# Kernel tuning notes

Hardware: AMD Instinct MI355X
Metric: run time of the kernel (lower is better)

Reference implementation:

```python
import jax, jax.numpy as jnp
import numpy as np

D_MODEL = 2048
NUM_HEADS = 16
D_K = D_MODEL // NUM_HEADS  # 128
MAX_SEQ_LEN = 4096
THETA = 10000.0
BATCH = 2
SEQ = 2048


def _trunc_normal(key, shape, std):
    # approximate trunc_normal_(mean=0, std, a=-3std, b=3std)
    return jnp.clip(jax.random.normal(key, shape) * std, -3 * std, 3 * std)


def setup_inputs() -> dict:
    key = jax.random.key(0)
    k0, k1, k2, k3, k4 = jax.random.split(key, 5)
    std = 2.0 / (D_MODEL + D_MODEL) ** 0.5
    in_features = jax.random.normal(k0, (BATCH, SEQ, D_MODEL), dtype=jnp.float32)
    token_positions = jnp.arange(SEQ, dtype=jnp.int64 if jax.config.jax_enable_x64 else jnp.int32)
    wq = _trunc_normal(k1, (D_MODEL, D_MODEL), std)
    wk = _trunc_normal(k2, (D_MODEL, D_MODEL), std)
    wv = _trunc_normal(k3, (D_MODEL, D_MODEL), std)
    wo = _trunc_normal(k4, (D_MODEL, D_MODEL), std)
    return {"in_features": in_features, "token_positions": token_positions,
            "wq": wq, "wk": wk, "wv": wv, "wo": wo}


def _rope(x, token_positions):
    # x: [b, h, s, d_k]; token_positions: [s]
    freqs = 1.0 / THETA ** (jnp.arange(0, D_K, 2, dtype=jnp.float32) / D_K)  # [d_k/2]
    angles = token_positions.astype(jnp.float32)[:, None] * freqs[None, :]   # [s, d_k/2]
    sin = jnp.sin(angles)
    cos = jnp.cos(angles)
    x1 = x[..., ::2]
    x2 = x[..., 1::2]
    rot = jnp.stack([x1 * cos - x2 * sin, x1 * sin + x2 * cos], axis=-1)  # [b,h,s,d_k/2,2]
    return rot.reshape(x.shape)


def reference(in_features, token_positions, wq, wk, wv, wo):
    b, s, _ = in_features.shape
    # projections: weight is [d_out, d_in]
    q = jnp.einsum('oi,bsi->bso', wq, in_features)
    k = jnp.einsum('oi,bsi->bso', wk, in_features)
    v = jnp.einsum('oi,bsi->bso', wv, in_features)
    # split heads: [b, s, h*d] -> [b, h, s, d]
    def split(t):
        return t.reshape(b, s, NUM_HEADS, D_K).transpose(0, 2, 1, 3)
    q, k, v = split(q), split(k), split(v)
    q = _rope(q, token_positions)
    k = _rope(k, token_positions)
    scores = jnp.einsum('bhqd,bhkd->bhqk', q, k) / jnp.sqrt(jnp.float32(D_K))
    causal = jnp.tril(jnp.ones((s, s), dtype=bool))
    scores = jnp.where(causal, scores, -jnp.inf)
    attn = jax.nn.softmax(scores, axis=-1)
    out = jnp.einsum('bhqk,bhkd->bhqd', attn, v)
    out = out.transpose(0, 2, 1, 3).reshape(b, s, D_MODEL)
    return jnp.einsum('oi,bsi->bso', wo, out)
```

## Files before the change

### kernel.cpp

```cpp
#include <hip/hip_runtime.h>
#include <cstdint>

typedef unsigned short u16;
typedef __attribute__((ext_vector_type(8))) short short8;
typedef __attribute__((ext_vector_type(4))) float f32x4;
typedef __attribute__((ext_vector_type(16))) float f32x16;
typedef __attribute__((ext_vector_type(2))) unsigned int uint2v;

#define D_MODEL 2048
#define NHEAD   16
#define DK      128
#define SEQQ    2048
#define BATCH   2
#define MTOT    (BATCH*SEQQ)

#define FENCE() asm volatile("" ::: "memory")
#define BARRIER() do { FENCE(); __builtin_amdgcn_s_barrier(); FENCE(); } while (0)

__device__ __forceinline__ u16 f2b(float f) {
  union { float f; uint32_t u; } c; c.f = f;
  uint32_t u = c.u;
  u += 0x7fffu + ((u >> 16) & 1u);
  return (u16)(u >> 16);
}
__device__ __forceinline__ float b2f(u16 h) {
  union { uint32_t u; float f; } c; c.u = ((uint32_t)h) << 16;
  return c.f;
}

__device__ __forceinline__ void gload_lds16(const void* g, void* l) {
  __builtin_amdgcn_global_load_lds(
      (const __attribute__((address_space(1))) void*)(uintptr_t)g,
      (__attribute__((address_space(3))) void*)(uint32_t)(uintptr_t)l,
      16, 0, 0);
}

__global__ __launch_bounds__(256) void cvt_bf16(const float* __restrict__ src,
                                                u16* __restrict__ dst, int n4) {
  int i = blockIdx.x * 256 + threadIdx.x;
  if (i >= n4) return;
  float4 v = ((const float4*)src)[i];
  union { u16 s[4]; uint64_t q; } o;
  o.s[0] = f2b(v.x); o.s[1] = f2b(v.y); o.s[2] = f2b(v.z); o.s[3] = f2b(v.w);
  ((uint64_t*)dst)[i] = o.q;
}

__global__ __launch_bounds__(256) void cvt_w(const float* __restrict__ wq,
                                             const float* __restrict__ wk,
                                             const float* __restrict__ wv,
                                             const float* __restrict__ wo,
                                             u16* __restrict__ Wqkv,
                                             u16* __restrict__ Wob) {
  int i = blockIdx.x * 256 + threadIdx.x;
  int which = i >> 20, j = i & 1048575;
  const float* src = (which == 0) ? wq : (which == 1) ? wk : (which == 2) ? wv : wo;
  u16* dst = (which < 3) ? (Wqkv + (size_t)which * 4194304) : Wob;
  float4 v = ((const float4*)src)[j];
  union { u16 s[4]; uint64_t q; } o;
  o.s[0] = f2b(v.x); o.s[1] = f2b(v.y); o.s[2] = f2b(v.z); o.s[3] = f2b(v.w);
  ((uint64_t*)dst)[j] = o.q;
}

template<int MODE>
__global__ __launch_bounds__(512) void gemm8(const u16* __restrict__ A,
                                             const u16* __restrict__ B,
                                             u16* __restrict__ Cq, u16* __restrict__ Ck,
                                             u16* __restrict__ Vt, float* __restrict__ Cf,
                                             int cpx) {
  __shared__ __align__(16) u16 As[3][128 * 64];
  __shared__ __align__(16) u16 Bs[3][256 * 64];
  const int tid = threadIdx.x;
  const int wave = tid >> 6, lane = tid & 63;
  const int l15 = lane & 15, l4 = lane >> 4;
  const int wr = wave >> 2, wc = wave & 3;
  const int wg = ((int)blockIdx.x & 7) * cpx + ((int)blockIdx.x >> 3);
  const int bm = wg & 31, bn = wg >> 5;
  const int row0 = bm * 128, col0 = bn * 256;

  const u16* asrc[2]; const u16* bsrc[4];
  {
    const int r = tid >> 3, c8 = tid & 7;
#pragma unroll
    for (int p = 0; p < 2; ++p) {
      int row = p * 64 + r;
      asrc[p] = A + (size_t)(row0 + row) * 2048 + ((c8 ^ (row & 7)) << 3);
    }
#pragma unroll
    for (int p = 0; p < 4; ++p) {
      int row = p * 64 + r;
      bsrc[p] = B + (size_t)(col0 + row) * 2048 + ((c8 ^ (row & 7)) << 3);
    }
  }
  const int ldst = wave * 512 + lane * 8;

  int aoff[4][2], boff[4][2];
#pragma unroll
  for (int m = 0; m < 4; ++m) {
    int row = wr * 64 + m * 16 + l15;
#pragma unroll
    for (int ks = 0; ks < 2; ++ks)
      aoff[m][ks] = row * 64 + (((ks * 4 + l4) ^ (l15 & 7)) << 3);
  }
#pragma unroll
  for (int n = 0; n < 4; ++n) {
    int row = wc * 64 + n * 16 + l15;
#pragma unroll
    for (int ks = 0; ks < 2; ++ks)
      boff[n][ks] = row * 64 + (((ks * 4 + l4) ^ (l15 & 7)) << 3);
  }

  f32x4 acc[4][4] = {};

#define STAGE0(slot, kt) do { \
    gload_lds16(asrc[0] + ((kt) << 6), &As[slot][0 * 4096 + ldst]); \
    gload_lds16(asrc[1] + ((kt) << 6), &As[slot][1 * 4096 + ldst]); \
    gload_lds16(bsrc[0] + ((kt) << 6), &Bs[slot][0 * 4096 + ldst]); \
  } while (0)
#define STAGE1(slot, kt) do { \
    gload_lds16(bsrc[1] + ((kt) << 6), &Bs[slot][1 * 4096 + ldst]); \
    gload_lds16(bsrc[2] + ((kt) << 6), &Bs[slot][2 * 4096 + ldst]); \
    gload_lds16(bsrc[3] + ((kt) << 6), &Bs[slot][3 * 4096 + ldst]); \
  } while (0)

  STAGE0(0, 0); STAGE1(0, 0);
  STAGE0(1, 1); STAGE1(1, 1);
  asm volatile("s_waitcnt vmcnt(6)" ::: "memory");
  BARRIER();

  int slot = 0;
  for (int t = 0; t < 32; ++t) {
    const int slot2 = slot ? slot - 1 : 2;
    const bool pf = (t + 2 < 32);
    short8 af[4], bf[4];
#pragma unroll
    for (int m = 0; m < 4; ++m) af[m] = *(const short8*)&As[slot][aoff[m][0]];
#pragma unroll
    for (int n = 0; n < 4; ++n) bf[n] = *(const short8*)&Bs[slot][boff[n][0]];
    if (pf) STAGE0(slot2, t + 2);
    BARRIER();
    __builtin_amdgcn_s_setprio(1);
#pragma unroll
    for (int m = 0; m < 4; ++m)
#pragma unroll
      for (int n = 0; n < 4; ++n)
        acc[m][n] = __builtin_amdgcn_mfma_f32_16x16x32_bf16(af[m], bf[n], acc[m][n], 0, 0, 0);
    __builtin_amdgcn_s_setprio(0);
    BARRIER();
#pragma unroll
    for (int m = 0; m < 4; ++m) af[m] = *(const short8*)&As[slot][aoff[m][1]];
#pragma unroll
    for (int n = 0; n < 4; ++n) bf[n] = *(const short8*)&Bs[slot][boff[n][1]];
    if (pf) STAGE1(slot2, t + 2);
    BARRIER();
    __builtin_amdgcn_s_setprio(1);
#pragma unroll
    for (int m = 0; m < 4; ++m)
#pragma unroll
      for (int n = 0; n < 4; ++n)
        acc[m][n] = __builtin_amdgcn_mfma_f32_16x16x32_bf16(af[m], bf[n], acc[m][n], 0, 0, 0);
    __builtin_amdgcn_s_setprio(0);
    if (pf) asm volatile("s_waitcnt vmcnt(6)" ::: "memory");
    else    asm volatile("s_waitcnt vmcnt(0)" ::: "memory");
    BARRIER();
    slot = (slot == 2) ? 0 : slot + 1;
  }
#undef STAGE0
#undef STAGE1

#pragma unroll
  for (int m = 0; m < 4; ++m) {
    const int row = row0 + wr * 64 + m * 16 + l4 * 4;
#pragma unroll
    for (int n = 0; n < 4; ++n) {
      const int col = wc * 64 + n * 16 + l15;
      if (MODE == 1) {
#pragma unroll
        for (int r = 0; r < 4; ++r)
          Cf[(size_t)(row + r) * 2048 + col0 + col] = acc[m][n][r];
      } else {
        const int region = col0 >> 11;
        const int col2 = (col0 & 2047) + col;
        if (region < 2) {
          u16* Cx = region ? Ck : Cq;
#pragma unroll
          for (int r = 0; r < 4; ++r)
            Cx[(size_t)(row + r) * 2048 + col2] = f2b(acc[m][n][r]);
        } else {
          union { u16 h4[4]; uint64_t q; } pk;
#pragma unroll
          for (int r = 0; r < 4; ++r) pk.h4[r] = f2b(acc[m][n][r]);
          const int bb = row >> 11, ss = row & 2047;
          const int hh = col2 >> 7, dd = col2 & 127;
          *(uint64_t*)&Vt[((size_t)((bb << 4) + hh) * 128 + dd) * 2048 + ss] = pk.q;
        }
      }
    }
  }
}

__global__ __launch_bounds__(256) void rope_qk(u16* __restrict__ Qb, u16* __restrict__ Kb,
                                               const int* __restrict__ pos) {
  int p = blockIdx.x * 256 + threadIdx.x;
  u16* X = (p >> 22) ? Kb : Qb;
  int pp = p & 4194303;
  int m = pp >> 10, j2 = pp & 1023;
  int h = j2 >> 6, j = j2 & 63;
  int s = m & (SEQQ - 1);
  float fp = (float)pos[s];
  float freq = exp2f((float)j * -0.20762050593046014f);
  float ang = fp * freq;
  float sn, cs;
  sincosf(ang, &sn, &cs);
  u16* px = X + (size_t)m * D_MODEL + h * DK + 2 * j;
  uint32_t pair = *(uint32_t*)px;
  float x1 = b2f((u16)(pair & 0xffff)), x2 = b2f((u16)(pair >> 16));
  u16 r1 = f2b(x1 * cs - x2 * sn);
  u16 r2 = f2b(x1 * sn + x2 * cs);
  *(uint32_t*)px = (uint32_t)r1 | ((uint32_t)r2 << 16);
}

__global__ __launch_bounds__(256) void attn_fwd(const u16* __restrict__ Q,
                                                const u16* __restrict__ Kg,
                                                const u16* __restrict__ Vt,
                                                u16* __restrict__ O) {
  __shared__ __align__(16) u16 Klds[2][64 * 128];
  __shared__ __align__(16) u16 Vlds[2][128 * 64];
  const int tid = threadIdx.x, wave = tid >> 6, lane = tid & 63;
  const int l31 = lane & 31, l5 = lane >> 5;
  const int bh = blockIdx.x;
  const int bxr = 15 - (int)blockIdx.y;
  const int b = bh >> 4, h = bh & 15;
  const int q0 = bxr * 128, qw = q0 + wave * 32;
  const float qscale = 0.1275174470974136f;

  short8 bq[8];
  {
    const u16* Qp = Q + (size_t)(b * SEQQ + qw + l31) * D_MODEL + h * DK + l5 * 8;
#pragma unroll
    for (int dt = 0; dt < 8; ++dt) {
      short8 raw = *(const short8*)(Qp + dt * 16);
#pragma unroll
      for (int j = 0; j < 8; ++j) raw[j] = (short)f2b(b2f((u16)raw[j]) * qscale);
      bq[dt] = raw;
    }
  }
  asm volatile("s_waitcnt vmcnt(0)" ::: "memory");

  f32x16 facc[4] = {};
  float mrun = -1e30f, lpart = 0.f;

  const u16* Kbase = Kg + (size_t)b * SEQQ * D_MODEL + h * DK;
  const u16* Vbase = Vt + (size_t)bh * DK * SEQQ;
  const u16* ksrc[4]; const u16* vsrc[4];
#pragma unroll
  for (int g = 0; g < 4; ++g) {
    int kr = g * 16 + (tid >> 4);
    int kc = ((tid & 15) * 8) ^ ((kr & 7) << 3);
    ksrc[g] = Kbase + (size_t)kr * D_MODEL + kc;
    int vr = g * 32 + (tid >> 3);
    int vc = ((tid & 7) * 8) ^ ((vr & 7) << 3);
    vsrc[g] = Vbase + (size_t)vr * SEQQ + vc;
  }
  const int dstoff = tid * 8;
  const int nkt = 2 * (bxr + 1);

#pragma unroll
  for (int g = 0; g < 4; ++g) { gload_lds16(ksrc[g], &Klds[0][g * 2048 + dstoff]); ksrc[g] += (size_t)64 * D_MODEL; }
#pragma unroll
  for (int g = 0; g < 4; ++g) { gload_lds16(vsrc[g], &Vlds[0][g * 2048 + dstoff]); vsrc[g] += 64; }

  for (int kt = 0; kt < nkt; ++kt) {
    const int k0 = kt * 64, cur = kt & 1;
    asm volatile("s_waitcnt vmcnt(0)" ::: "memory");
    BARRIER();
    if (kt + 1 < nkt) {
#pragma unroll
      for (int g = 0; g < 4; ++g) { gload_lds16(ksrc[g], &Klds[cur ^ 1][g * 2048 + dstoff]); ksrc[g] += (size_t)64 * D_MODEL; }
#pragma unroll
      for (int g = 0; g < 4; ++g) { gload_lds16(vsrc[g], &Vlds[cur ^ 1][g * 2048 + dstoff]); vsrc[g] += 64; }
    }
    if (k0 > qw + 31) continue;

    const u16* Kl = Klds[cur];
    const u16* Vl = Vlds[cur];

    f32x16 st0 = {}, st1 = {};
    __builtin_amdgcn_s_setprio(1);
#pragma unroll
    for (int dt = 0; dt < 8; ++dt) {
      const int ch = ((2 * dt + l5) ^ (l31 & 7)) * 8;
      short8 ak0 = *(const short8*)&Kl[l31 * 128 + ch];
      short8 ak1 = *(const short8*)&Kl[(32 + l31) * 128 + ch];
      st0 = __builtin_amdgcn_mfma_f32_32x32x16_bf16(ak0, bq[dt], st0, 0, 0, 0);
      st1 = __builtin_amdgcn_mfma_f32_32x32x16_bf16(ak1, bq[dt], st1, 0, 0, 0);
    }
    __builtin_amdgcn_s_setprio(0);

    if (k0 + 63 > qw) {
      const int qm = qw + l31 - k0 - 4 * l5;
#pragma unroll
      for (int r = 0; r < 16; ++r) {
        const int kc0 = (r & 3) + 8 * (r >> 2);
        st0[r] = (kc0 > qm) ? -1e30f : st0[r];
        st1[r] = (kc0 + 32 > qm) ? -1e30f : st1[r];
      }
    }

    float mx[8];
#pragma unroll
    for (int r = 0; r < 8; ++r) mx[r] = fmaxf(fmaxf(st0[r], st0[r + 8]), fmaxf(st1[r], st1[r + 8]));
    float m = fmaxf(fmaxf(fmaxf(mx[0], mx[1]), fmaxf(mx[2], mx[3])),
                    fmaxf(fmaxf(mx[4], mx[5]), fmaxf(mx[6], mx[7])));
    {
      uint2v sw = __builtin_amdgcn_permlane32_swap(__float_as_uint(m), __float_as_uint(m), false, false);
      m = fmaxf(__uint_as_float(sw.x), __uint_as_float(sw.y));
    }
    const float mn = fmaxf(mrun, m);
    const float al = exp2f(mrun - mn);
    mrun = mn;
    float ps = 0.f;
#pragma unroll
    for (int r = 0; r < 16; ++r) { float p = exp2f(st0[r] - mn); st0[r] = p; ps += p; }
#pragma unroll
    for (int r = 0; r < 16; ++r) { float p = exp2f(st1[r] - mn); st1[r] = p; ps += p; }
    lpart = lpart * al + ps;
#pragma unroll
    for (int db = 0; db < 4; ++db) facc[db] *= al;

    short8 pa[4];
#pragma unroll
    for (int ks2 = 0; ks2 < 2; ++ks2) {
#pragma unroll
      for (int t0 = 0; t0 < 2; ++t0) {
        uint32_t c0w0, c0w1, c1w0, c1w1;
        if (ks2 == 0) {
          asm("v_cvt_pk_bf16_f32 %0, %1, %2" : "=v"(c0w0) : "v"(st0[8 * t0 + 0]), "v"(st0[8 * t0 + 1]));
          asm("v_cvt_pk_bf16_f32 %0, %1, %2" : "=v"(c0w1) : "v"(st0[8 * t0 + 2]), "v"(st0[8 * t0 + 3]));
          asm("v_cvt_pk_bf16_f32 %0, %1, %2" : "=v"(c1w0) : "v"(st0[8 * t0 + 4]), "v"(st0[8 * t0 + 5]));
          asm("v_cvt_pk_bf16_f32 %0, %1, %2" : "=v"(c1w1) : "v"(st0[8 * t0 + 6]), "v"(st0[8 * t0 + 7]));
        } else {
          asm("v_cvt_pk_bf16_f32 %0, %1, %2" : "=v"(c0w0) : "v"(st1[8 * t0 + 0]), "v"(st1[8 * t0 + 1]));
          asm("v_cvt_pk_bf16_f32 %0, %1, %2" : "=v"(c0w1) : "v"(st1[8 * t0 + 2]), "v"(st1[8 * t0 + 3]));
          asm("v_cvt_pk_bf16_f32 %0, %1, %2" : "=v"(c1w0) : "v"(st1[8 * t0 + 4]), "v"(st1[8 * t0 + 5]));
          asm("v_cvt_pk_bf16_f32 %0, %1, %2" : "=v"(c1w1) : "v"(st1[8 * t0 + 6]), "v"(st1[8 * t0 + 7]));
        }
        uint2v s0 = __builtin_amdgcn_permlane32_swap(c0w0, c1w0, false, false);
        uint2v s1 = __builtin_amdgcn_permlane32_swap(c0w1, c1w1, false, false);
        union { uint32_t w[4]; short8 v; } u;
        u.w[0] = s0.x; u.w[1] = s1.x; u.w[2] = s0.y; u.w[3] = s1.y;
        pa[2 * ks2 + t0] = u.v;
      }
    }

    __builtin_amdgcn_s_setprio(1);
#pragma unroll
    for (int db = 0; db < 4; ++db) {
      const int row = 32 * db + l31;
#pragma unroll
      for (int t = 0; t < 4; ++t) {
        const int ch = ((2 * t + l5) ^ (l31 & 7)) * 8;
        short8 av = *(const short8*)&Vl[row * 64 + ch];
        facc[db] = __builtin_amdgcn_mfma_f32_32x32x16_bf16(av, pa[t], facc[db], 0, 0, 0);
      }
    }
    __builtin_amdgcn_s_setprio(0);
  }

  float inv;
  {
    uint2v sw = __builtin_amdgcn_permlane32_swap(__float_as_uint(lpart), __float_as_uint(lpart), false, false);
    inv = 1.0f / (__uint_as_float(sw.x) + __uint_as_float(sw.y));
  }
  u16* Op = O + (size_t)(b * SEQQ + qw + l31) * D_MODEL + h * DK;
#pragma unroll
  for (int db = 0; db < 4; ++db)
#pragma unroll
    for (int a = 0; a < 4; ++a) {
      union { u16 h4[4]; uint64_t q; } pk;
#pragma unroll
      for (int c = 0; c < 4; ++c) pk.h4[c] = f2b(facc[db][4 * a + c] * inv);
      *(uint64_t*)&Op[32 * db + 8 * a + 4 * l5] = pk.q;
    }
}

extern "C" void kernel_launch(void* const* d_in, const int* in_sizes, int n_in,
                              void* d_out, int out_size, void* d_ws, size_t ws_size,
                              hipStream_t stream) {
  const float* x   = (const float*)d_in[0];
  const int*   pos = (const int*)d_in[1];
  const float* wq  = (const float*)d_in[2];
  const float* wk  = (const float*)d_in[3];
  const float* wv  = (const float*)d_in[4];
  const float* wo  = (const float*)d_in[5];
  float* out = (float*)d_out;
  char* ws = (char*)d_ws;

  u16* Xb   = (u16*)(ws);
  u16* Wqkv = (u16*)(ws + (16u << 20));
  u16* Wob  = (u16*)(ws + (40u << 20));
  u16* Qb   = (u16*)(ws + (48u << 20));
  u16* Kb   = (u16*)(ws + (64u << 20));
  u16* Vt   = (u16*)(ws + (80u << 20));
  u16* AO   = Xb;

  const int nX = MTOT * D_MODEL;

  cvt_bf16<<<nX / 1024, 256, 0, stream>>>(x, Xb, nX / 4);
  cvt_w<<<16384, 256, 0, stream>>>(wq, wk, wv, wo, Wqkv, Wob);

  gemm8<0><<<768, 512, 0, stream>>>(Xb, Wqkv, Qb, Kb, Vt, nullptr, 96);

  rope_qk<<<32768, 256, 0, stream>>>(Qb, Kb, pos);

  attn_fwd<<<dim3(BATCH * NHEAD, SEQQ / 128), 256, 0, stream>>>(Qb, Kb, Vt, AO);

  gemm8<1><<<256, 512, 0, stream>>>(AO, Wob, nullptr, nullptr, nullptr, out, 32);
}
```

Baseline: 276.6 us.

## Templatize GEMM tile height and switch to simple double-buffered pipeline

The GEMM kernel is now templated on M-fragments. The QKV projection uses 256x256 tiles (384 blocks), and the output projection keeps 128x256. The triple-buffered, split-phase schedule with explicit vmcnt waits and four barriers per iteration becomes a double buffer with one __syncthreads per k-step, and all of a step's loads are issued up front. Larger QKV tiles raise operand reuse and cut global traffic, but they use more registers and LDS and give fewer blocks. The simpler sync may expose more load latency, and no explicit wait for the async LDS loads is visible before they are read.

```diff
diff --git a/kernel.cpp b/kernel.cpp
--- a/kernel.cpp
+++ b/kernel.cpp
@@ -61,42 +61,44 @@
   ((uint64_t*)dst)[j] = o.q;
 }
 
-template<int MODE>
-__global__ __launch_bounds__(512) void gemm8(const u16* __restrict__ A,
+template<int MF, int MODE>
+__global__ __launch_bounds__(512) void gemmT(const u16* __restrict__ A,
                                              const u16* __restrict__ B,
                                              u16* __restrict__ Cq, u16* __restrict__ Ck,
                                              u16* __restrict__ Vt, float* __restrict__ Cf,
-                                             int cpx) {
-  __shared__ __align__(16) u16 As[3][128 * 64];
-  __shared__ __align__(16) u16 Bs[3][256 * 64];
+                                             int nbm, int cpx) {
+  constexpr int BM = MF * 32;
+  constexpr int AG = BM / 64;
+  __shared__ __align__(16) u16 As[2][BM * 64];
+  __shared__ __align__(16) u16 Bs[2][256 * 64];
   const int tid = threadIdx.x;
   const int wave = tid >> 6, lane = tid & 63;
   const int l15 = lane & 15, l4 = lane >> 4;
   const int wr = wave >> 2, wc = wave & 3;
   const int wg = ((int)blockIdx.x & 7) * cpx + ((int)blockIdx.x >> 3);
-  const int bm = wg & 31, bn = wg >> 5;
-  const int row0 = bm * 128, col0 = bn * 256;
-
-  const u16* asrc[2]; const u16* bsrc[4];
+  const int bm = wg % nbm, bn = wg / nbm;
+  const int row0 = bm * BM, col0 = bn * 256;
+
+  const u16* asrc[AG]; const u16* bsrc[4];
   {
     const int r = tid >> 3, c8 = tid & 7;
 #pragma unroll
-    for (int p = 0; p < 2; ++p) {
-      int row = p * 64 + r;
-      asrc[p] = A + (size_t)(row0 + row) * 2048 + ((c8 ^ (row & 7)) << 3);
-    }
-#pragma unroll
-    for (int p = 0; p < 4; ++p) {
-      int row = p * 64 + r;
-      bsrc[p] = B + (size_t)(col0 + row) * 2048 + ((c8 ^ (row & 7)) << 3);
-    }
-  }
-  const int ldst = wave * 512 + lane * 8;
-
-  int aoff[4][2], boff[4][2];
-#pragma unroll
-  for (int m = 0; m < 4; ++m) {
-    int row = wr * 64 + m * 16 + l15;
+    for (int g = 0; g < AG; ++g) {
+      int row = g * 64 + r;
+      asrc[g] = A + (size_t)(row0 + row) * 2048 + ((c8 ^ (row & 7)) << 3);
+    }
+#pragma unroll
+    for (int g = 0; g < 4; ++g) {
+      int row = g * 64 + r;
+      bsrc[g] = B + (size_t)(col0 + row) * 2048 + ((c8 ^ (row & 7)) << 3);
+    }
+  }
+  const int ldst = tid * 8;
+
+  int aoff[MF][2], boff[4][2];
+#pragma unroll
+  for (int m = 0; m < MF; ++m) {
+    int row = wr * (MF * 16) + m * 16 + l15;
 #pragma unroll
     for (int ks = 0; ks < 2; ++ks)
       aoff[m][ks] = row * 64 + (((ks * 4 + l4) ^ (l15 & 7)) << 3);
@@ -109,67 +111,53 @@
       boff[n][ks] = row * 64 + (((ks * 4 + l4) ^ (l15 & 7)) << 3);
   }
 
-  f32x4 acc[4][4] = {};
-
-#define STAGE0(slot, kt) do { \
-    gload_lds16(asrc[0] + ((kt) << 6), &As[slot][0 * 4096 + ldst]); \
-    gload_lds16(asrc[1] + ((kt) << 6), &As[slot][1 * 4096 + ldst]); \
-    gload_lds16(bsrc[0] + ((kt) << 6), &Bs[slot][0 * 4096 + ldst]); \
-  } while (0)
-#define STAGE1(slot, kt) do { \
-    gload_lds16(bsrc[1] + ((kt) << 6), &Bs[slot][1 * 4096 + ldst]); \
-    gload_lds16(bsrc[2] + ((kt) << 6), &Bs[slot][2 * 4096 + ldst]); \
-    gload_lds16(bsrc[3] + ((kt) << 6), &Bs[slot][3 * 4096 + ldst]); \
-  } while (0)
-
-  STAGE0(0, 0); STAGE1(0, 0);
-  STAGE0(1, 1); STAGE1(1, 1);
-  asm volatile("s_waitcnt vmcnt(6)" ::: "memory");
-  BARRIER();
-
-  int slot = 0;
+  f32x4 acc[MF][4] = {};
+
+  {
+#pragma unroll
+    for (int g = 0; g < AG; ++g) gload_lds16(asrc[g], &As[0][g * 4096 + ldst]);
+#pragma unroll
+    for (int g = 0; g < 4; ++g)  gload_lds16(bsrc[g], &Bs[0][g * 4096 + ldst]);
+  }
+
   for (int t = 0; t < 32; ++t) {
-    const int slot2 = slot ? slot - 1 : 2;
-    const bool pf = (t + 2 < 32);
-    short8 af[4], bf[4];
-#pragma unroll
-    for (int m = 0; m < 4; ++m) af[m] = *(const short8*)&As[slot][aoff[m][0]];
-#pragma unroll
-    for (int n = 0; n < 4; ++n) bf[n] = *(const short8*)&Bs[slot][boff[n][0]];
-    if (pf) STAGE0(slot2, t + 2);
-    BARRIER();
-    __builtin_amdgcn_s_setprio(1);
-#pragma unroll
-    for (int m = 0; m < 4; ++m)
+    const int buf = t & 1;
+    __syncthreads();
+    if (t + 1 < 32) {
+#pragma unroll
+      for (int g = 0; g < AG; ++g) gload_lds16(asrc[g] + ((t + 1) << 6), &As[buf ^ 1][g * 4096 + ldst]);
+#pragma unroll
+      for (int g = 0; g < 4; ++g)  gload_lds16(bsrc[g] + ((t + 1) << 6), &Bs[buf ^ 1][g * 4096 + ldst]);
+    }
+    short8 bfr[4][2];
+#pragma unroll
+    for (int n = 0; n < 4; ++n)
+#pragma unroll
+      for (int ks = 0; ks < 2; ++ks)
+        bfr[n][ks] = *(const short8*)&Bs[buf][boff[n][ks]];
+#pragma unroll
+    for (int p = 0; p < MF / 2; ++p) {
+      short8 a0[2], a1[2];
+#pragma unroll
+      for (int ks = 0; ks < 2; ++ks) {
+        a0[ks] = *(const short8*)&As[buf][aoff[2 * p][ks]];
+        a1[ks] = *(const short8*)&As[buf][aoff[2 * p + 1][ks]];
+      }
+      __builtin_amdgcn_s_setprio(1);
 #pragma unroll
       for (int n = 0; n < 4; ++n)
-        acc[m][n] = __builtin_amdgcn_mfma_f32_16x16x32_bf16(af[m], bf[n], acc[m][n], 0, 0, 0);
-    __builtin_amdgcn_s_setprio(0);
-    BARRIER();
-#pragma unroll
-    for (int m = 0; m < 4; ++m) af[m] = *(const short8*)&As[slot][aoff[m][1]];
-#pragma unroll
-    for (int n = 0; n < 4; ++n) bf[n] = *(const short8*)&Bs[slot][boff[n][1]];
-    if (pf) STAGE1(slot2, t + 2);
-    BARRIER();
-    __builtin_amdgcn_s_setprio(1);
-#pragma unroll
-    for (int m = 0; m < 4; ++m)
-#pragma unroll
-      for (int n = 0; n < 4; ++n)
-        acc[m][n] = __builtin_amdgcn_mfma_f32_16x16x32_bf16(af[m], bf[n], acc[m][n], 0, 0, 0);
-    __builtin_amdgcn_s_setprio(0);
-    if (pf) asm volatile("s_waitcnt vmcnt(6)" ::: "memory");
-    else    asm volatile("s_waitcnt vmcnt(0)" ::: "memory");
-    BARRIER();
-    slot = (slot == 2) ? 0 : slot + 1;
-  }
-#undef STAGE0
-#undef STAGE1
-
-#pragma unroll
-  for (int m = 0; m < 4; ++m) {
-    const int row = row0 + wr * 64 + m * 16 + l4 * 4;
+#pragma unroll
+        for (int ks = 0; ks < 2; ++ks) {
+          acc[2 * p][n]     = __builtin_amdgcn_mfma_f32_16x16x32_bf16(a0[ks], bfr[n][ks], acc[2 * p][n], 0, 0, 0);
+          acc[2 * p + 1][n] = __builtin_amdgcn_mfma_f32_16x16x32_bf16(a1[ks], bfr[n][ks], acc[2 * p + 1][n], 0, 0, 0);
+        }
+      __builtin_amdgcn_s_setprio(0);
+    }
+  }
+
+#pragma unroll
+  for (int m = 0; m < MF; ++m) {
+    const int row = row0 + wr * (MF * 16) + m * 16 + l4 * 4;
 #pragma unroll
     for (int n = 0; n < 4; ++n) {
       const int col = wc * 64 + n * 16 + l15;
@@ -408,11 +396,11 @@
   cvt_bf16<<<nX / 1024, 256, 0, stream>>>(x, Xb, nX / 4);
   cvt_w<<<16384, 256, 0, stream>>>(wq, wk, wv, wo, Wqkv, Wob);
 
-  gemm8<0><<<768, 512, 0, stream>>>(Xb, Wqkv, Qb, Kb, Vt, nullptr, 96);
+  gemmT<8, 0><<<384, 512, 0, stream>>>(Xb, Wqkv, Qb, Kb, Vt, nullptr, 16, 48);
 
   rope_qk<<<32768, 256, 0, stream>>>(Qb, Kb, pos);
 
   attn_fwd<<<dim3(BATCH * NHEAD, SEQQ / 128), 256, 0, stream>>>(Qb, Kb, Vt, AO);
 
-  gemm8<1><<<256, 512, 0, stream>>>(AO, Wob, nullptr, nullptr, nullptr, out, 32);
-}
+  gemmT<4, 1><<<256, 512, 0, stream>>>(AO, Wob, nullptr, nullptr, nullptr, out, 32, 32);
+}
```

Result: no change. 275.7 us (-0.3%).
